# Performance work log

Hardware: AMD Instinct MI355X
Metric: run time of the kernel (lower is better)

Reference implementation:

```python
import jax, jax.numpy as jnp
import numpy as np

LATENT_DIM = 8
HALF = LATENT_DIM // 2
N_BLOCKS = 3
EPS = 1e-10


def _causal_graphs(koopman):
    # koopman: [C, D, D] real. Batched eig-decomp, band-pass eigenvalues by |lam| in [0.9, 1.1],
    # equivalent to selecting stable columns/rows: V_s diag(lam_s) V_s^-1 == V diag(lam*mask) V^-1.
    lam, V = jnp.linalg.eig(koopman)            # lam: [C,D] complex, V: [C,D,D]
    Vinv = jnp.linalg.inv(V)
    lam = lam + (1e-10 + 1e-10j)
    a = jnp.abs(lam)
    mask = (a <= 1.1) & (a >= 0.9)              # [C,D]
    # fallback: if no stable eigenvalue in a group, keep all (torch.arange branch)
    mask = jnp.where(jnp.any(mask, axis=-1, keepdims=True), mask, True)
    lam_m = lam * mask.astype(lam.dtype)
    G = jnp.einsum('cij,cj,cjk->cik', V, lam_m, Vinv)
    return jnp.real(G).astype(koopman.dtype)    # [C,D,D]


def _coupling(x, cond, W0, b0, W1, b1, W2, b2):
    # Conditional affine coupling flow: x,cond [..., D]. Returns (z, logdet [...])
    logdet = jnp.zeros(x.shape[:-1], dtype=x.dtype)
    for i in range(N_BLOCKS):
        x1, x2 = x[..., :HALF], x[..., HALF:]
        if i % 2 == 1:
            x1, x2 = x2, x1
        h = jnp.concatenate([x1, cond], axis=-1)            # [..., HALF + D]
        h = jax.nn.relu(h @ W0[i] + b0[i])
        h = jax.nn.relu(h @ W1[i] + b1[i])
        o = h @ W2[i] + b2[i]                               # [..., 2*HALF]
        s = jnp.tanh(o[..., :HALF])
        t = o[..., HALF:]
        x2 = x2 * jnp.exp(s) + t
        logdet = logdet + jnp.sum(s, axis=-1)
        if i % 2 == 1:
            x1, x2 = x2, x1
        x = jnp.concatenate([x1, x2], axis=-1)
    return x, logdet


def _std_normal_logprob(z):
    # standard MVN log prob, summed over last dim
    D = z.shape[-1]
    c = jnp.asarray(0.5 * D * np.log(2.0 * np.pi), dtype=z.dtype)
    return -0.5 * jnp.sum(z * z, axis=-1) - c


def setup_inputs() -> dict:
    key = jax.random.key(0)
    ks = jax.random.split(key, 9)
    B, N, T, D, C, H = 32, 4096, 16, LATENT_DIM, 32, 64
    latent = jax.random.normal(ks[0], (B, N, T, D), dtype=jnp.float32)
    # scale so eigenvalue magnitudes cluster near ~1 (spectral radius of D x D gaussian ~ 0.35*sqrt(D))
    koopman_tilde = jax.random.normal(ks[1], (C, D, D), dtype=jnp.float32) * 0.35
    community = jax.random.normal(ks[2], (N, C), dtype=jnp.float32)
    s0 = 1.0 / np.sqrt(HALF + D)
    s1 = 1.0 / np.sqrt(H)
    W0 = jax.random.normal(ks[3], (N_BLOCKS, HALF + D, H), dtype=jnp.float32) * s0
    b0 = jnp.zeros((N_BLOCKS, H), dtype=jnp.float32)
    W1 = jax.random.normal(ks[4], (N_BLOCKS, H, H), dtype=jnp.float32) * s1
    b1 = jnp.zeros((N_BLOCKS, H), dtype=jnp.float32)
    W2 = jax.random.normal(ks[5], (N_BLOCKS, H, 2 * HALF), dtype=jnp.float32) * s1
    b2 = jnp.zeros((N_BLOCKS, 2 * HALF), dtype=jnp.float32)
    return {"latent": latent, "koopman_tilde": koopman_tilde, "community": community,
            "W0": W0, "b0": b0, "W1": W1, "b1": b1, "W2": W2, "b2": b2}


def reference(latent, koopman_tilde, community, W0, b0, W1, b1, W2, b2):
    # scale_type == 'community' branch
    community_class = jnp.argmax(community, axis=-1)        # [N], topk k=1 indices
    graphs = _causal_graphs(koopman_tilde)                  # [C, D, D]
    G_node = graphs[community_class]                        # [N, D, D] gather per node
    # dispatch/matmul/combine fused as one einsum (parent[:, class==i] = latent[:, class==i] @ G_i)
    parent = jnp.einsum('bntd,nde->bnte', latent, G_node)
    ez, logdet = _coupling(latent, parent, W0, b0, W1, b1, W2, b2)
    log_pz = _std_normal_logprob(ez) + logdet               # [B, N, T]
    return log_pz
```

## Files before the change

kernel.cpp:

```cpp
#include <hip/hip_runtime.h>
#include <hip/hip_bf16.h>

typedef __attribute__((ext_vector_type(8))) short     bf16x8;
typedef __attribute__((ext_vector_type(4))) float     f32x4;
typedef __attribute__((ext_vector_type(4))) unsigned  u32x4;

__device__ inline unsigned short bf16_rn(float x) {
  unsigned u = __float_as_uint(x);
  unsigned r = (u + 0x7FFFu + ((u >> 16) & 1u)) >> 16;
  return (unsigned short)r;
}
__device__ inline unsigned cvt_pk_bf16(float a, float b) {
  unsigned r;
  asm("v_cvt_pk_bf16_f32 %0, %1, %2" : "=v"(r) : "v"(a), "v"(b));
  return r;
}
__device__ inline void pin4f(f32x4& v) { asm("" : "+v"(v)); }
__device__ inline void pin4u(u32x4& v) { asm("" : "+v"(v)); }
__device__ inline void wfence() {
  asm volatile("s_waitcnt lgkmcnt(0)" ::: "memory");
}
__device__ inline float tanh_fast(float v) {
  float vv = fminf(fmaxf(v, -15.f), 15.f);
  float e = __expf(2.f * vv);
  return (e - 1.f) * __builtin_amdgcn_rcpf(e + 1.f);
}

__global__ __launch_bounds__(256) void prologue_kernel(
    const float* __restrict__ Kt, const float* __restrict__ comm,
    const float* __restrict__ W0, const float* __restrict__ W1,
    const float* __restrict__ W2,
    float* __restrict__ Gout, int* __restrict__ cls,
    unsigned* __restrict__ wfrag)
{
  const int b = blockIdx.x;
  const int t = threadIdx.x;

  if (b < 32) {
    __shared__ double Kd[64];
    __shared__ double Pw[2][64];
    __shared__ double psum[8];
    __shared__ double coefs[9];
    __shared__ double rts[16];
    __shared__ double Gpart[64][8];

    const int tl = t & 63;
    const int row = tl >> 3, col = tl & 7;

    if (t < 64) Kd[tl] = (double)Kt[b * 64 + tl];
    __syncthreads();
    if (t < 64) Pw[0][tl] = Kd[tl];
    __syncthreads();

    int cur = 0;
    for (int p = 1; p <= 8; ++p) {
      if (t == 0) {
        double tr = 0.0;
        for (int d = 0; d < 8; ++d) tr += Pw[cur][d * 9];
        psum[p - 1] = tr;
      }
      if (p < 8 && t < 64) {
        double sacc = 0.0;
        for (int k = 0; k < 8; ++k) sacc += Pw[cur][row * 8 + k] * Kd[k * 8 + col];
        Pw[cur ^ 1][tl] = sacc;
      }
      __syncthreads();
      cur ^= 1;
    }

    if (t == 0) {
      double a[9];
      a[0] = 1.0;
      for (int k = 1; k <= 8; ++k) {
        double ssum = psum[k - 1];
        for (int i = 1; i < k; ++i) ssum += a[i] * psum[k - i - 1];
        a[k] = -ssum / (double)k;
      }
      for (int k = 0; k <= 8; ++k) coefs[k] = a[k];
    }
    __syncthreads();

    if (t < 8) {
      double a8[9];
      #pragma unroll
      for (int k = 0; k <= 8; ++k) a8[k] = coefs[k];
      double zre = 1.0, zim = 0.0;
      for (int q = 0; q <= t; ++q) {
        double t1 = zre * 0.4 - zim * 0.9;
        double t2 = zre * 0.9 + zim * 0.4;
        zre = t1; zim = t2;
      }
      for (int it = 0; it < 40; ++it) {
        double pre = a8[0], pim = 0.0;
        #pragma unroll
        for (int k = 1; k <= 8; ++k) {
          double t1 = pre * zre - pim * zim + a8[k];
          double t2 = pre * zim + pim * zre;
          pre = t1; pim = t2;
        }
        double dre = 1.0, dim = 0.0;
        for (int j = 0; j < 8; ++j) {
          double ore = __shfl(zre, j, 64);
          double oim = __shfl(zim, j, 64);
          if (j != t) {
            double sre = zre - ore, sim = zim - oim;
            double t1 = dre * sre - dim * sim;
            double t2 = dre * sim + dim * sre;
            dre = t1; dim = t2;
          }
        }
        double d2 = dre * dre + dim * dim;
        if (d2 < 1e-60) d2 = 1e-60;
        double qre = (pre * dre + pim * dim) / d2;
        double qim = (pim * dre - pre * dim) / d2;
        zre -= qre; zim -= qim;
      }
      rts[t] = zre; rts[8 + t] = zim;
    }
    __syncthreads();

    if (t < 64) {
      double lre[8], lim[8];
      #pragma unroll
      for (int j = 0; j < 8; ++j) { lre[j] = rts[j]; lim[j] = rts[8 + j]; }

      bool keep[8]; bool any = false;
      #pragma unroll
      for (int j = 0; j < 8; ++j) {
        double sre = lre[j] + 1e-10, sim = lim[j] + 1e-10;
        double amod = sqrt(sre * sre + sim * sim);
        keep[j] = (amod <= 1.1) && (amod >= 0.9);
        any = any || keep[j];
      }
      #pragma unroll
      for (int j = 0; j < 8; ++j) if (!any) keep[j] = true;

      const int r = tl >> 3, myrow = tl & 7;
      const int first = (r == 0) ? 1 : 0;
      double vre[8], vim[8];
      #pragma unroll
      for (int cc = 0; cc < 8; ++cc) {
        vre[cc] = Kd[myrow * 8 + cc] - ((myrow == cc) ? lre[first] : 0.0);
        vim[cc] = (myrow == cc) ? -lim[first] : 0.0;
      }
      #pragma unroll
      for (int j = 0; j < 8; ++j) {
        if (j == r || j == first) continue;
        double nre[8], nim[8];
        #pragma unroll
        for (int cc = 0; cc < 8; ++cc) {
          double are = 0.0, aim = 0.0;
          #pragma unroll
          for (int k = 0; k < 8; ++k) {
            double bre = Kd[k * 8 + cc] - ((k == cc) ? lre[j] : 0.0);
            double bim = (k == cc) ? -lim[j] : 0.0;
            are += vre[k] * bre - vim[k] * bim;
            aim += vre[k] * bim + vim[k] * bre;
          }
          nre[cc] = are; nim[cc] = aim;
        }
        #pragma unroll
        for (int cc = 0; cc < 8; ++cc) { vre[cc] = nre[cc]; vim[cc] = nim[cc]; }
      }

      double dre = 1.0, dim = 0.0;
      #pragma unroll
      for (int j = 0; j < 8; ++j) {
        if (j == r) continue;
        double ure = lre[r] - lre[j], uim = lim[r] - lim[j];
        double t1 = dre * ure - dim * uim;
        double t2 = dre * uim + dim * ure;
        dre = t1; dim = t2;
      }
      double numre = keep[r] ? (lre[r] + 1e-10) : 0.0;
      double numim = keep[r] ? (lim[r] + 1e-10) : 0.0;
      double dd = dre * dre + dim * dim;
      if (dd < 1e-300) dd = 1e-300;
      double cre = (numre * dre + numim * dim) / dd;
      double cim = (numim * dre - numre * dim) / dd;

      #pragma unroll
      for (int cc = 0; cc < 8; ++cc)
        Gpart[tl][cc] = cre * vre[cc] - cim * vim[cc];
    }
    __syncthreads();

    if (t < 64) {
      double sum = 0.0;
      #pragma unroll
      for (int rr = 0; rr < 8; ++rr) sum += Gpart[rr * 8 + (t >> 3)][t & 7];
      Gout[b * 64 + t] = (float)sum;
    }
    return;
  }

  if (b < 48) {
    int n = (b - 32) * 256 + t;
    if (n < 4096) {
      const float* rowp = comm + n * 32;
      float best = rowp[0];
      int bi = 0;
      #pragma unroll
      for (int c = 1; c < 32; ++c) {
        float v = rowp[c];
        if (v > best) { best = v; bi = c; }
      }
      cls[n] = bi;
    }
    return;
  }

  {
    int gid = (b - 48) * 256 + t;
    if (gid >= 42 * 64) return;
    int fid = gid >> 6, lane = gid & 63;
    int i = fid / 14, fl = fid % 14;
    int c = lane & 15, g = lane >> 4;

    unsigned short vals[8];
    #pragma unroll
    for (int j = 0; j < 8; ++j) {
      float v = 0.f;
      if (fl < 4) {
        int nb = fl;
        int k = 8 * g + j;
        if (k < 12) v = W0[i * 768 + k * 64 + 16 * nb + c];
      } else if (fl < 12) {
        int q = fl - 4; int kb = q >> 2, nb = q & 3;
        int k = 32 * kb + 16 * ((j >> 2) & 1) + 4 * g + 2 * ((j >> 1) & 1) + (j & 1);
        v = W1[i * 4096 + k * 64 + 16 * nb + c];
      } else {
        int kb = fl - 12;
        int k = 32 * kb + 16 * ((j >> 2) & 1) + 4 * g + 2 * ((j >> 1) & 1) + (j & 1);
        if (c < 8) v = W2[i * 512 + k * 8 + c];
      }
      vals[j] = bf16_rn(v);
    }
    u32x4 o;
    #pragma unroll
    for (int tt = 0; tt < 4; ++tt)
      o[tt] = (unsigned)vals[2 * tt] | ((unsigned)vals[2 * tt + 1] << 16);
    *(u32x4*)(wfrag + fid * 256 + lane * 4) = o;
  }
}

#define SPB 256

__global__ __launch_bounds__(256, 2) void causal_mfma_kernel(
    const float* __restrict__ latent, const float* __restrict__ graphs,
    const int* __restrict__ cls, const unsigned* __restrict__ wfrag,
    const float* __restrict__ b0, const float* __restrict__ b1,
    const float* __restrict__ b2, float* __restrict__ out)
{
  __shared__ unsigned wsh[42 * 256];
  __shared__ float    bsh[408];
  __shared__ char     ex[4][2048];

  const int t = threadIdx.x;
  const int lane = t & 63;
  const int w = t >> 6;
  const int c = lane & 15;
  const int g = lane >> 4;
  const int s = blockIdx.x * SPB + t;
  char* my = ex[w];

  #pragma unroll
  for (int q = 0; q < 11; ++q) {
    int idx = q * 256 + t;
    if (idx < 42 * 64)
      *(u32x4*)(wsh + idx * 4) = *(const u32x4*)(wfrag + idx * 4);
  }
  for (int idx = t; idx < 408; idx += 256) {
    bsh[idx] = (idx < 192) ? b0[idx] : (idx < 384) ? b1[idx - 192] : b2[idx - 384];
  }

  float x[8];
  {
    const float4 xa = *(const float4*)(latent + (size_t)s * 8);
    const float4 xb = *(const float4*)(latent + (size_t)s * 8 + 4);
    x[0] = xa.x; x[1] = xa.y; x[2] = xa.z; x[3] = xa.w;
    x[4] = xb.x; x[5] = xb.y; x[6] = xb.z; x[7] = xb.w;
  }
  unsigned parP0, parP1;
  u32x4 hi4;
  {
    float par[8];
    const int n = (s >> 4) & 4095;
    const float* G = graphs + cls[n] * 64;
    #pragma unroll
    for (int e = 0; e < 8; ++e) par[e] = 0.f;
    #pragma unroll
    for (int d = 0; d < 8; ++d) {
      const float xd = x[d];
      const float4 g0 = *(const float4*)(G + d * 8);
      const float4 g1 = *(const float4*)(G + d * 8 + 4);
      par[0] += xd * g0.x; par[1] += xd * g0.y; par[2] += xd * g0.z; par[3] += xd * g0.w;
      par[4] += xd * g1.x; par[5] += xd * g1.y; par[6] += xd * g1.z; par[7] += xd * g1.w;
    }
    parP0 = cvt_pk_bf16(par[0], par[1]);
    parP1 = cvt_pk_bf16(par[2], par[3]);
    hi4[0] = cvt_pk_bf16(par[4], par[5]);
    hi4[1] = cvt_pk_bf16(par[6], par[7]);
    hi4[2] = 0u; hi4[3] = 0u;
  }

  __syncthreads();

  const char* wl = (const char*)wsh + lane * 16;
  char* a_u  = my + lane * 32;
  char* a_b0 = my + (c)      * 32 + g * 16;
  char* a_b1 = my + (16 + c) * 32 + g * 16;
  char* a_b2 = my + (32 + c) * 32 + g * 16;
  char* a_b3 = my + (48 + c) * 32 + g * 16;

  float logdet = 0.f;

  #pragma unroll
  for (int i = 0; i < 3; ++i) {
    const int in0 = (i & 1) ? 4 : 0;
    const int tr0 = (i & 1) ? 0 : 4;
    const char* wbase = wl + (size_t)(i * 14) * 1024;

    {
      u32x4 lo4;
      lo4[0] = cvt_pk_bf16(x[in0], x[in0 + 1]);
      lo4[1] = cvt_pk_bf16(x[in0 + 2], x[in0 + 3]);
      lo4[2] = parP0; lo4[3] = parP1;
      wfence();
      *(u32x4*)a_u = lo4;
      *(u32x4*)(a_u + 16) = hi4;
      wfence();
    }

    u32x4 B1[4];
    {
      u32x4 z = {0u, 0u, 0u, 0u};
      B1[0] = (g < 2) ? *(const u32x4*)a_b0 : z;
      B1[1] = (g < 2) ? *(const u32x4*)a_b1 : z;
      B1[2] = (g < 2) ? *(const u32x4*)a_b2 : z;
      B1[3] = (g < 2) ? *(const u32x4*)a_b3 : z;
      pin4u(B1[0]); pin4u(B1[1]); pin4u(B1[2]); pin4u(B1[3]);
    }

    u32x4 B2k0[4], B2k1[4];
    {
      f32x4 a0[4], a1[4];
      bf16x8 A0 = *(const bf16x8*)(wbase + 0 * 1024);
      bf16x8 A1 = *(const bf16x8*)(wbase + 1 * 1024);
      f32x4 bv0 = *(const f32x4*)(bsh + i * 64 + 0 * 16 + g * 4);
      f32x4 bv1 = *(const f32x4*)(bsh + i * 64 + 1 * 16 + g * 4);
      #pragma unroll
      for (int mb = 0; mb < 4; ++mb) {
        a0[mb] = __builtin_amdgcn_mfma_f32_16x16x32_bf16(
            A0, __builtin_bit_cast(bf16x8, B1[mb]), bv0, 0, 0, 0);
        pin4f(a0[mb]);
      }
      #pragma unroll
      for (int mb = 0; mb < 4; ++mb) {
        a1[mb] = __builtin_amdgcn_mfma_f32_16x16x32_bf16(
            A1, __builtin_bit_cast(bf16x8, B1[mb]), bv1, 0, 0, 0);
        pin4f(a1[mb]);
      }
      #pragma unroll
      for (int mb = 0; mb < 4; ++mb) {
        B2k0[mb] = u32x4{cvt_pk_bf16(fmaxf(a0[mb][0], 0.f), fmaxf(a0[mb][1], 0.f)),
                         cvt_pk_bf16(fmaxf(a0[mb][2], 0.f), fmaxf(a0[mb][3], 0.f)),
                         cvt_pk_bf16(fmaxf(a1[mb][0], 0.f), fmaxf(a1[mb][1], 0.f)),
                         cvt_pk_bf16(fmaxf(a1[mb][2], 0.f), fmaxf(a1[mb][3], 0.f))};
        pin4u(B2k0[mb]);
      }
    }
    {
      f32x4 a0[4], a1[4];
      bf16x8 A0 = *(const bf16x8*)(wbase + 2 * 1024);
      bf16x8 A1 = *(const bf16x8*)(wbase + 3 * 1024);
      f32x4 bv0 = *(const f32x4*)(bsh + i * 64 + 2 * 16 + g * 4);
      f32x4 bv1 = *(const f32x4*)(bsh + i * 64 + 3 * 16 + g * 4);
      #pragma unroll
      for (int mb = 0; mb < 4; ++mb) {
        a0[mb] = __builtin_amdgcn_mfma_f32_16x16x32_bf16(
            A0, __builtin_bit_cast(bf16x8, B1[mb]), bv0, 0, 0, 0);
        pin4f(a0[mb]);
      }
      #pragma unroll
      for (int mb = 0; mb < 4; ++mb) {
        a1[mb] = __builtin_amdgcn_mfma_f32_16x16x32_bf16(
            A1, __builtin_bit_cast(bf16x8, B1[mb]), bv1, 0, 0, 0);
        pin4f(a1[mb]);
      }
      #pragma unroll
      for (int mb = 0; mb < 4; ++mb) {
        B2k1[mb] = u32x4{cvt_pk_bf16(fmaxf(a0[mb][0], 0.f), fmaxf(a0[mb][1], 0.f)),
                         cvt_pk_bf16(fmaxf(a0[mb][2], 0.f), fmaxf(a0[mb][3], 0.f)),
                         cvt_pk_bf16(fmaxf(a1[mb][0], 0.f), fmaxf(a1[mb][1], 0.f)),
                         cvt_pk_bf16(fmaxf(a1[mb][2], 0.f), fmaxf(a1[mb][3], 0.f))};
        pin4u(B2k1[mb]);
      }
    }

    u32x4 B3k0[4], B3k1[4];
    {
      f32x4 a0[4], a1[4];
      bf16x8 Ak0n0 = *(const bf16x8*)(wbase + (4 + 0) * 1024);
      bf16x8 Ak0n1 = *(const bf16x8*)(wbase + (4 + 1) * 1024);
      bf16x8 Ak1n0 = *(const bf16x8*)(wbase + (8 + 0) * 1024);
      bf16x8 Ak1n1 = *(const bf16x8*)(wbase + (8 + 1) * 1024);
      f32x4 bv0 = *(const f32x4*)(bsh + 192 + i * 64 + 0 * 16 + g * 4);
      f32x4 bv1 = *(const f32x4*)(bsh + 192 + i * 64 + 1 * 16 + g * 4);
      #pragma unroll
      for (int mb = 0; mb < 4; ++mb) {
        a0[mb] = __builtin_amdgcn_mfma_f32_16x16x32_bf16(
            Ak0n0, __builtin_bit_cast(bf16x8, B2k0[mb]), bv0, 0, 0, 0);
        a0[mb] = __builtin_amdgcn_mfma_f32_16x16x32_bf16(
            Ak1n0, __builtin_bit_cast(bf16x8, B2k1[mb]), a0[mb], 0, 0, 0);
        pin4f(a0[mb]);
      }
      #pragma unroll
      for (int mb = 0; mb < 4; ++mb) {
        a1[mb] = __builtin_amdgcn_mfma_f32_16x16x32_bf16(
            Ak0n1, __builtin_bit_cast(bf16x8, B2k0[mb]), bv1, 0, 0, 0);
        a1[mb] = __builtin_amdgcn_mfma_f32_16x16x32_bf16(
            Ak1n1, __builtin_bit_cast(bf16x8, B2k1[mb]), a1[mb], 0, 0, 0);
        pin4f(a1[mb]);
      }
      #pragma unroll
      for (int mb = 0; mb < 4; ++mb) {
        B3k0[mb] = u32x4{cvt_pk_bf16(fmaxf(a0[mb][0], 0.f), fmaxf(a0[mb][1], 0.f)),
                         cvt_pk_bf16(fmaxf(a0[mb][2], 0.f), fmaxf(a0[mb][3], 0.f)),
                         cvt_pk_bf16(fmaxf(a1[mb][0], 0.f), fmaxf(a1[mb][1], 0.f)),
                         cvt_pk_bf16(fmaxf(a1[mb][2], 0.f), fmaxf(a1[mb][3], 0.f))};
        pin4u(B3k0[mb]);
      }
    }
    {
      f32x4 a0[4], a1[4];
      bf16x8 Ak0n2 = *(const bf16x8*)(wbase + (4 + 2) * 1024);
      bf16x8 Ak0n3 = *(const bf16x8*)(wbase + (4 + 3) * 1024);
      bf16x8 Ak1n2 = *(const bf16x8*)(wbase + (8 + 2) * 1024);
      bf16x8 Ak1n3 = *(const bf16x8*)(wbase + (8 + 3) * 1024);
      f32x4 bv0 = *(const f32x4*)(bsh + 192 + i * 64 + 2 * 16 + g * 4);
      f32x4 bv1 = *(const f32x4*)(bsh + 192 + i * 64 + 3 * 16 + g * 4);
      #pragma unroll
      for (int mb = 0; mb < 4; ++mb) {
        a0[mb] = __builtin_amdgcn_mfma_f32_16x16x32_bf16(
            Ak0n2, __builtin_bit_cast(bf16x8, B2k0[mb]), bv0, 0, 0, 0);
        a0[mb] = __builtin_amdgcn_mfma_f32_16x16x32_bf16(
            Ak1n2, __builtin_bit_cast(bf16x8, B2k1[mb]), a0[mb], 0, 0, 0);
        pin4f(a0[mb]);
      }
      #pragma unroll
      for (int mb = 0; mb < 4; ++mb) {
        a1[mb] = __builtin_amdgcn_mfma_f32_16x16x32_bf16(
            Ak0n3, __builtin_bit_cast(bf16x8, B2k0[mb]), bv1, 0, 0, 0);
        a1[mb] = __builtin_amdgcn_mfma_f32_16x16x32_bf16(
            Ak1n3, __builtin_bit_cast(bf16x8, B2k1[mb]), a1[mb], 0, 0, 0);
        pin4f(a1[mb]);
      }
      #pragma unroll
      for (int mb = 0; mb < 4; ++mb) {
        B3k1[mb] = u32x4{cvt_pk_bf16(fmaxf(a0[mb][0], 0.f), fmaxf(a0[mb][1], 0.f)),
                         cvt_pk_bf16(fmaxf(a0[mb][2], 0.f), fmaxf(a0[mb][3], 0.f)),
                         cvt_pk_bf16(fmaxf(a1[mb][0], 0.f), fmaxf(a1[mb][1], 0.f)),
                         cvt_pk_bf16(fmaxf(a1[mb][2], 0.f), fmaxf(a1[mb][3], 0.f))};
        pin4u(B3k1[mb]);
      }
    }

    f32x4 acc3[4];
    {
      bf16x8 A0 = *(const bf16x8*)(wbase + 12 * 1024);
      bf16x8 A1 = *(const bf16x8*)(wbase + 13 * 1024);
      f32x4 z = {0.f, 0.f, 0.f, 0.f};
      f32x4 bC2 = (g < 2) ? *(const f32x4*)(bsh + 384 + i * 8 + g * 4) : z;
      #pragma unroll
      for (int mb = 0; mb < 4; ++mb) {
        f32x4 tmp = __builtin_amdgcn_mfma_f32_16x16x32_bf16(
            A0, __builtin_bit_cast(bf16x8, B3k0[mb]), bC2, 0, 0, 0);
        acc3[mb] = __builtin_amdgcn_mfma_f32_16x16x32_bf16(
            A1, __builtin_bit_cast(bf16x8, B3k1[mb]), tmp, 0, 0, 0);
        pin4f(acc3[mb]);
      }
    }

    wfence();
    if (g < 2) {
      *(u32x4*)a_b0 = __builtin_bit_cast(u32x4, acc3[0]);
      *(u32x4*)a_b1 = __builtin_bit_cast(u32x4, acc3[1]);
      *(u32x4*)a_b2 = __builtin_bit_cast(u32x4, acc3[2]);
      *(u32x4*)a_b3 = __builtin_bit_cast(u32x4, acc3[3]);
    }
    wfence();

    {
      u32x4 o0 = *(const u32x4*)a_u;
      u32x4 o1 = *(const u32x4*)(a_u + 16);
      float sv0 = tanh_fast(__uint_as_float(o0[0]));
      float sv1 = tanh_fast(__uint_as_float(o0[1]));
      float sv2 = tanh_fast(__uint_as_float(o0[2]));
      float sv3 = tanh_fast(__uint_as_float(o0[3]));
      x[tr0 + 0] = x[tr0 + 0] * __expf(sv0) + __uint_as_float(o1[0]);
      x[tr0 + 1] = x[tr0 + 1] * __expf(sv1) + __uint_as_float(o1[1]);
      x[tr0 + 2] = x[tr0 + 2] * __expf(sv2) + __uint_as_float(o1[2]);
      x[tr0 + 3] = x[tr0 + 3] * __expf(sv3) + __uint_as_float(o1[3]);
      logdet += sv0 + sv1 + sv2 + sv3;
    }
  }

  float ss = 0.f;
  #pragma unroll
  for (int q = 0; q < 8; ++q) ss += x[q] * x[q];
  out[s] = -0.5f * ss - 7.3515082656373810f + logdet;
}

extern "C" void kernel_launch(void* const* d_in, const int* in_sizes, int n_in,
                              void* d_out, int out_size, void* d_ws, size_t ws_size,
                              hipStream_t stream) {
  const float* latent  = (const float*)d_in[0];
  const float* koopman = (const float*)d_in[1];
  const float* comm    = (const float*)d_in[2];
  const float* W0      = (const float*)d_in[3];
  const float* b0      = (const float*)d_in[4];
  const float* W1      = (const float*)d_in[5];
  const float* b1      = (const float*)d_in[6];
  const float* W2      = (const float*)d_in[7];
  const float* b2      = (const float*)d_in[8];
  float* out = (float*)d_out;

  float*    graphs_ws = (float*)d_ws;
  int*      cls_ws    = (int*)((char*)d_ws + 8192);
  unsigned* wfrag_ws  = (unsigned*)((char*)d_ws + 24576);

  prologue_kernel<<<59, 256, 0, stream>>>(
      koopman, comm, W0, W1, W2, graphs_ws, cls_ws, wfrag_ws);

  const int total = 32 * 4096 * 16;
  causal_mfma_kernel<<<total / SPB, SPB, 0, stream>>>(
      latent, graphs_ws, cls_ws, wfrag_ws, b0, b1, b2, out);
}
```

Before: 149.9 us.

## Process two sample tiles per thread to interleave independent MFMA chains

Each 256-thread block now handles 512 samples: every thread carries two independent samples through the three coupling blocks, with a second per-wave LDS exchange buffer. MFMA calls for the two tiles are interleaved so the dependent accumulate chains overlap, weight fragments loaded from LDS are reused across both tiles, and the per-block weight staging cost is spread over twice the work. In exchange register pressure roughly doubles, which at launch bounds (256,2) risks spills, and the grid shrinks by half.

```diff
diff --git a/kernel.cpp b/kernel.cpp
--- a/kernel.cpp
+++ b/kernel.cpp
@@ -24,6 +24,9 @@
   float vv = fminf(fmaxf(v, -15.f), 15.f);
   float e = __expf(2.f * vv);
   return (e - 1.f) * __builtin_amdgcn_rcpf(e + 1.f);
+}
+__device__ inline unsigned rp(float a, float b) {
+  return cvt_pk_bf16(fmaxf(a, 0.f), fmaxf(b, 0.f));
 }
 
 __global__ __launch_bounds__(256) void prologue_kernel(
@@ -244,7 +247,7 @@
   }
 }
 
-#define SPB 256
+#define SPB 512
 
 __global__ __launch_bounds__(256, 2) void causal_mfma_kernel(
     const float* __restrict__ latent, const float* __restrict__ graphs,
@@ -254,15 +257,18 @@
 {
   __shared__ unsigned wsh[42 * 256];
   __shared__ float    bsh[408];
-  __shared__ char     ex[4][2048];
+  __shared__ char     ex0[4][2048];
+  __shared__ char     ex1[4][2048];
 
   const int t = threadIdx.x;
   const int lane = t & 63;
   const int w = t >> 6;
   const int c = lane & 15;
   const int g = lane >> 4;
-  const int s = blockIdx.x * SPB + t;
-  char* my = ex[w];
+  const int s0 = blockIdx.x * SPB + t;
+  const int s1 = s0 + 256;
+  char* my0 = ex0[w];
+  char* my1 = ex1[w];
 
   #pragma unroll
   for (int q = 0; q < 11; ++q) {
@@ -274,46 +280,73 @@
     bsh[idx] = (idx < 192) ? b0[idx] : (idx < 384) ? b1[idx - 192] : b2[idx - 384];
   }
 
-  float x[8];
+  float xA[8], xB[8];
   {
-    const float4 xa = *(const float4*)(latent + (size_t)s * 8);
-    const float4 xb = *(const float4*)(latent + (size_t)s * 8 + 4);
-    x[0] = xa.x; x[1] = xa.y; x[2] = xa.z; x[3] = xa.w;
-    x[4] = xb.x; x[5] = xb.y; x[6] = xb.z; x[7] = xb.w;
-  }
-  unsigned parP0, parP1;
-  u32x4 hi4;
+    const float4 a0 = *(const float4*)(latent + (size_t)s0 * 8);
+    const float4 a1 = *(const float4*)(latent + (size_t)s0 * 8 + 4);
+    xA[0] = a0.x; xA[1] = a0.y; xA[2] = a0.z; xA[3] = a0.w;
+    xA[4] = a1.x; xA[5] = a1.y; xA[6] = a1.z; xA[7] = a1.w;
+    const float4 b0v = *(const float4*)(latent + (size_t)s1 * 8);
+    const float4 b1v = *(const float4*)(latent + (size_t)s1 * 8 + 4);
+    xB[0] = b0v.x; xB[1] = b0v.y; xB[2] = b0v.z; xB[3] = b0v.w;
+    xB[4] = b1v.x; xB[5] = b1v.y; xB[6] = b1v.z; xB[7] = b1v.w;
+  }
+  unsigned pA0, pA1, pB0, pB1;
+  u32x4 hiA, hiB;
   {
     float par[8];
-    const int n = (s >> 4) & 4095;
-    const float* G = graphs + cls[n] * 64;
+    const float* G = graphs + cls[(s0 >> 4) & 4095] * 64;
     #pragma unroll
     for (int e = 0; e < 8; ++e) par[e] = 0.f;
     #pragma unroll
     for (int d = 0; d < 8; ++d) {
-      const float xd = x[d];
+      const float xd = xA[d];
       const float4 g0 = *(const float4*)(G + d * 8);
       const float4 g1 = *(const float4*)(G + d * 8 + 4);
       par[0] += xd * g0.x; par[1] += xd * g0.y; par[2] += xd * g0.z; par[3] += xd * g0.w;
       par[4] += xd * g1.x; par[5] += xd * g1.y; par[6] += xd * g1.z; par[7] += xd * g1.w;
     }
-    parP0 = cvt_pk_bf16(par[0], par[1]);
-    parP1 = cvt_pk_bf16(par[2], par[3]);
-    hi4[0] = cvt_pk_bf16(par[4], par[5]);
-    hi4[1] = cvt_pk_bf16(par[6], par[7]);
-    hi4[2] = 0u; hi4[3] = 0u;
+    pA0 = cvt_pk_bf16(par[0], par[1]);
+    pA1 = cvt_pk_bf16(par[2], par[3]);
+    hiA[0] = cvt_pk_bf16(par[4], par[5]);
+    hiA[1] = cvt_pk_bf16(par[6], par[7]);
+    hiA[2] = 0u; hiA[3] = 0u;
+  }
+  {
+    float par[8];
+    const float* G = graphs + cls[(s1 >> 4) & 4095] * 64;
+    #pragma unroll
+    for (int e = 0; e < 8; ++e) par[e] = 0.f;
+    #pragma unroll
+    for (int d = 0; d < 8; ++d) {
+      const float xd = xB[d];
+      const float4 g0 = *(const float4*)(G + d * 8);
+      const float4 g1 = *(const float4*)(G + d * 8 + 4);
+      par[0] += xd * g0.x; par[1] += xd * g0.y; par[2] += xd * g0.z; par[3] += xd * g0.w;
+      par[4] += xd * g1.x; par[5] += xd * g1.y; par[6] += xd * g1.z; par[7] += xd * g1.w;
+    }
+    pB0 = cvt_pk_bf16(par[0], par[1]);
+    pB1 = cvt_pk_bf16(par[2], par[3]);
+    hiB[0] = cvt_pk_bf16(par[4], par[5]);
+    hiB[1] = cvt_pk_bf16(par[6], par[7]);
+    hiB[2] = 0u; hiB[3] = 0u;
   }
 
   __syncthreads();
 
   const char* wl = (const char*)wsh + lane * 16;
-  char* a_u  = my + lane * 32;
-  char* a_b0 = my + (c)      * 32 + g * 16;
-  char* a_b1 = my + (16 + c) * 32 + g * 16;
-  char* a_b2 = my + (32 + c) * 32 + g * 16;
-  char* a_b3 = my + (48 + c) * 32 + g * 16;
-
-  float logdet = 0.f;
+  char* aA_u  = my0 + lane * 32;
+  char* aA_b0 = my0 + (c)      * 32 + g * 16;
+  char* aA_b1 = my0 + (16 + c) * 32 + g * 16;
+  char* aA_b2 = my0 + (32 + c) * 32 + g * 16;
+  char* aA_b3 = my0 + (48 + c) * 32 + g * 16;
+  char* aB_u  = my1 + lane * 32;
+  char* aB_b0 = my1 + (c)      * 32 + g * 16;
+  char* aB_b1 = my1 + (16 + c) * 32 + g * 16;
+  char* aB_b2 = my1 + (32 + c) * 32 + g * 16;
+  char* aB_b3 = my1 + (48 + c) * 32 + g * 16;
+
+  float logdetA = 0.f, logdetB = 0.f;
 
   #pragma unroll
   for (int i = 0; i < 3; ++i) {
@@ -322,151 +355,197 @@
     const char* wbase = wl + (size_t)(i * 14) * 1024;
 
     {
-      u32x4 lo4;
-      lo4[0] = cvt_pk_bf16(x[in0], x[in0 + 1]);
-      lo4[1] = cvt_pk_bf16(x[in0 + 2], x[in0 + 3]);
-      lo4[2] = parP0; lo4[3] = parP1;
+      u32x4 loA, loB;
+      loA[0] = cvt_pk_bf16(xA[in0], xA[in0 + 1]);
+      loA[1] = cvt_pk_bf16(xA[in0 + 2], xA[in0 + 3]);
+      loA[2] = pA0; loA[3] = pA1;
+      loB[0] = cvt_pk_bf16(xB[in0], xB[in0 + 1]);
+      loB[1] = cvt_pk_bf16(xB[in0 + 2], xB[in0 + 3]);
+      loB[2] = pB0; loB[3] = pB1;
       wfence();
-      *(u32x4*)a_u = lo4;
-      *(u32x4*)(a_u + 16) = hi4;
+      *(u32x4*)aA_u = loA;
+      *(u32x4*)(aA_u + 16) = hiA;
+      *(u32x4*)aB_u = loB;
+      *(u32x4*)(aB_u + 16) = hiB;
       wfence();
     }
 
-    u32x4 B1[4];
+    u32x4 B1A[4], B1B[4];
     {
       u32x4 z = {0u, 0u, 0u, 0u};
-      B1[0] = (g < 2) ? *(const u32x4*)a_b0 : z;
-      B1[1] = (g < 2) ? *(const u32x4*)a_b1 : z;
-      B1[2] = (g < 2) ? *(const u32x4*)a_b2 : z;
-      B1[3] = (g < 2) ? *(const u32x4*)a_b3 : z;
-      pin4u(B1[0]); pin4u(B1[1]); pin4u(B1[2]); pin4u(B1[3]);
-    }
-
-    u32x4 B2k0[4], B2k1[4];
-    {
-      f32x4 a0[4], a1[4];
+      B1A[0] = (g < 2) ? *(const u32x4*)aA_b0 : z;
+      B1A[1] = (g < 2) ? *(const u32x4*)aA_b1 : z;
+      B1A[2] = (g < 2) ? *(const u32x4*)aA_b2 : z;
+      B1A[3] = (g < 2) ? *(const u32x4*)aA_b3 : z;
+      B1B[0] = (g < 2) ? *(const u32x4*)aB_b0 : z;
+      B1B[1] = (g < 2) ? *(const u32x4*)aB_b1 : z;
+      B1B[2] = (g < 2) ? *(const u32x4*)aB_b2 : z;
+      B1B[3] = (g < 2) ? *(const u32x4*)aB_b3 : z;
+      #pragma unroll
+      for (int mb = 0; mb < 4; ++mb) { pin4u(B1A[mb]); pin4u(B1B[mb]); }
+    }
+
+    u32x4 B2k0A[4], B2k1A[4], B2k0B[4], B2k1B[4];
+    {
       bf16x8 A0 = *(const bf16x8*)(wbase + 0 * 1024);
       bf16x8 A1 = *(const bf16x8*)(wbase + 1 * 1024);
       f32x4 bv0 = *(const f32x4*)(bsh + i * 64 + 0 * 16 + g * 4);
       f32x4 bv1 = *(const f32x4*)(bsh + i * 64 + 1 * 16 + g * 4);
-      #pragma unroll
-      for (int mb = 0; mb < 4; ++mb) {
-        a0[mb] = __builtin_amdgcn_mfma_f32_16x16x32_bf16(
-            A0, __builtin_bit_cast(bf16x8, B1[mb]), bv0, 0, 0, 0);
-        pin4f(a0[mb]);
-      }
-      #pragma unroll
-      for (int mb = 0; mb < 4; ++mb) {
-        a1[mb] = __builtin_amdgcn_mfma_f32_16x16x32_bf16(
-            A1, __builtin_bit_cast(bf16x8, B1[mb]), bv1, 0, 0, 0);
-        pin4f(a1[mb]);
-      }
-      #pragma unroll
-      for (int mb = 0; mb < 4; ++mb) {
-        B2k0[mb] = u32x4{cvt_pk_bf16(fmaxf(a0[mb][0], 0.f), fmaxf(a0[mb][1], 0.f)),
-                         cvt_pk_bf16(fmaxf(a0[mb][2], 0.f), fmaxf(a0[mb][3], 0.f)),
-                         cvt_pk_bf16(fmaxf(a1[mb][0], 0.f), fmaxf(a1[mb][1], 0.f)),
-                         cvt_pk_bf16(fmaxf(a1[mb][2], 0.f), fmaxf(a1[mb][3], 0.f))};
-        pin4u(B2k0[mb]);
-      }
-    }
-    {
-      f32x4 a0[4], a1[4];
+      f32x4 q0[4], q1[4], r0[4], r1[4];
+      #pragma unroll
+      for (int mb = 0; mb < 4; ++mb) {
+        q0[mb] = __builtin_amdgcn_mfma_f32_16x16x32_bf16(
+            A0, __builtin_bit_cast(bf16x8, B1A[mb]), bv0, 0, 0, 0);
+        pin4f(q0[mb]);
+        r0[mb] = __builtin_amdgcn_mfma_f32_16x16x32_bf16(
+            A0, __builtin_bit_cast(bf16x8, B1B[mb]), bv0, 0, 0, 0);
+        pin4f(r0[mb]);
+      }
+      #pragma unroll
+      for (int mb = 0; mb < 4; ++mb) {
+        q1[mb] = __builtin_amdgcn_mfma_f32_16x16x32_bf16(
+            A1, __builtin_bit_cast(bf16x8, B1A[mb]), bv1, 0, 0, 0);
+        pin4f(q1[mb]);
+        r1[mb] = __builtin_amdgcn_mfma_f32_16x16x32_bf16(
+            A1, __builtin_bit_cast(bf16x8, B1B[mb]), bv1, 0, 0, 0);
+        pin4f(r1[mb]);
+      }
+      #pragma unroll
+      for (int mb = 0; mb < 4; ++mb) {
+        B2k0A[mb] = u32x4{rp(q0[mb][0], q0[mb][1]), rp(q0[mb][2], q0[mb][3]),
+                          rp(q1[mb][0], q1[mb][1]), rp(q1[mb][2], q1[mb][3])};
+        pin4u(B2k0A[mb]);
+        B2k0B[mb] = u32x4{rp(r0[mb][0], r0[mb][1]), rp(r0[mb][2], r0[mb][3]),
+                          rp(r1[mb][0], r1[mb][1]), rp(r1[mb][2], r1[mb][3])};
+        pin4u(B2k0B[mb]);
+      }
+    }
+    {
       bf16x8 A0 = *(const bf16x8*)(wbase + 2 * 1024);
       bf16x8 A1 = *(const bf16x8*)(wbase + 3 * 1024);
       f32x4 bv0 = *(const f32x4*)(bsh + i * 64 + 2 * 16 + g * 4);
       f32x4 bv1 = *(const f32x4*)(bsh + i * 64 + 3 * 16 + g * 4);
-      #pragma unroll
-      for (int mb = 0; mb < 4; ++mb) {
-        a0[mb] = __builtin_amdgcn_mfma_f32_16x16x32_bf16(
-            A0, __builtin_bit_cast(bf16x8, B1[mb]), bv0, 0, 0, 0);
-        pin4f(a0[mb]);
-      }
-      #pragma unroll
-      for (int mb = 0; mb < 4; ++mb) {
-        a1[mb] = __builtin_amdgcn_mfma_f32_16x16x32_bf16(
-            A1, __builtin_bit_cast(bf16x8, B1[mb]), bv1, 0, 0, 0);
-        pin4f(a1[mb]);
-      }
-      #pragma unroll
-      for (int mb = 0; mb < 4; ++mb) {
-        B2k1[mb] = u32x4{cvt_pk_bf16(fmaxf(a0[mb][0], 0.f), fmaxf(a0[mb][1], 0.f)),
-                         cvt_pk_bf16(fmaxf(a0[mb][2], 0.f), fmaxf(a0[mb][3], 0.f)),
-                         cvt_pk_bf16(fmaxf(a1[mb][0], 0.f), fmaxf(a1[mb][1], 0.f)),
-                         cvt_pk_bf16(fmaxf(a1[mb][2], 0.f), fmaxf(a1[mb][3], 0.f))};
-        pin4u(B2k1[mb]);
-      }
-    }
-
-    u32x4 B3k0[4], B3k1[4];
-    {
-      f32x4 a0[4], a1[4];
+      f32x4 q0[4], q1[4], r0[4], r1[4];
+      #pragma unroll
+      for (int mb = 0; mb < 4; ++mb) {
+        q0[mb] = __builtin_amdgcn_mfma_f32_16x16x32_bf16(
+            A0, __builtin_bit_cast(bf16x8, B1A[mb]), bv0, 0, 0, 0);
+        pin4f(q0[mb]);
+        r0[mb] = __builtin_amdgcn_mfma_f32_16x16x32_bf16(
+            A0, __builtin_bit_cast(bf16x8, B1B[mb]), bv0, 0, 0, 0);
+        pin4f(r0[mb]);
+      }
+      #pragma unroll
+      for (int mb = 0; mb < 4; ++mb) {
+        q1[mb] = __builtin_amdgcn_mfma_f32_16x16x32_bf16(
+            A1, __builtin_bit_cast(bf16x8, B1A[mb]), bv1, 0, 0, 0);
+        pin4f(q1[mb]);
+        r1[mb] = __builtin_amdgcn_mfma_f32_16x16x32_bf16(
+            A1, __builtin_bit_cast(bf16x8, B1B[mb]), bv1, 0, 0, 0);
+        pin4f(r1[mb]);
+      }
+      #pragma unroll
+      for (int mb = 0; mb < 4; ++mb) {
+        B2k1A[mb] = u32x4{rp(q0[mb][0], q0[mb][1]), rp(q0[mb][2], q0[mb][3]),
+                          rp(q1[mb][0], q1[mb][1]), rp(q1[mb][2], q1[mb][3])};
+        pin4u(B2k1A[mb]);
+        B2k1B[mb] = u32x4{rp(r0[mb][0], r0[mb][1]), rp(r0[mb][2], r0[mb][3]),
+                          rp(r1[mb][0], r1[mb][1]), rp(r1[mb][2], r1[mb][3])};
+        pin4u(B2k1B[mb]);
+      }
+    }
+
+    u32x4 B3k0A[4], B3k1A[4], B3k0B[4], B3k1B[4];
+    {
       bf16x8 Ak0n0 = *(const bf16x8*)(wbase + (4 + 0) * 1024);
       bf16x8 Ak0n1 = *(const bf16x8*)(wbase + (4 + 1) * 1024);
       bf16x8 Ak1n0 = *(const bf16x8*)(wbase + (8 + 0) * 1024);
       bf16x8 Ak1n1 = *(const bf16x8*)(wbase + (8 + 1) * 1024);
       f32x4 bv0 = *(const f32x4*)(bsh + 192 + i * 64 + 0 * 16 + g * 4);
       f32x4 bv1 = *(const f32x4*)(bsh + 192 + i * 64 + 1 * 16 + g * 4);
-      #pragma unroll
-      for (int mb = 0; mb < 4; ++mb) {
-        a0[mb] = __builtin_amdgcn_mfma_f32_16x16x32_bf16(
-            Ak0n0, __builtin_bit_cast(bf16x8, B2k0[mb]), bv0, 0, 0, 0);
-        a0[mb] = __builtin_amdgcn_mfma_f32_16x16x32_bf16(
-            Ak1n0, __builtin_bit_cast(bf16x8, B2k1[mb]), a0[mb], 0, 0, 0);
-        pin4f(a0[mb]);
-      }
-      #pragma unroll
-      for (int mb = 0; mb < 4; ++mb) {
-        a1[mb] = __builtin_amdgcn_mfma_f32_16x16x32_bf16(
-            Ak0n1, __builtin_bit_cast(bf16x8, B2k0[mb]), bv1, 0, 0, 0);
-        a1[mb] = __builtin_amdgcn_mfma_f32_16x16x32_bf16(
-            Ak1n1, __builtin_bit_cast(bf16x8, B2k1[mb]), a1[mb], 0, 0, 0);
-        pin4f(a1[mb]);
-      }
-      #pragma unroll
-      for (int mb = 0; mb < 4; ++mb) {
-        B3k0[mb] = u32x4{cvt_pk_bf16(fmaxf(a0[mb][0], 0.f), fmaxf(a0[mb][1], 0.f)),
-                         cvt_pk_bf16(fmaxf(a0[mb][2], 0.f), fmaxf(a0[mb][3], 0.f)),
-                         cvt_pk_bf16(fmaxf(a1[mb][0], 0.f), fmaxf(a1[mb][1], 0.f)),
-                         cvt_pk_bf16(fmaxf(a1[mb][2], 0.f), fmaxf(a1[mb][3], 0.f))};
-        pin4u(B3k0[mb]);
-      }
-    }
-    {
-      f32x4 a0[4], a1[4];
+      f32x4 q0[4], q1[4], r0[4], r1[4];
+      #pragma unroll
+      for (int mb = 0; mb < 4; ++mb) {
+        q0[mb] = __builtin_amdgcn_mfma_f32_16x16x32_bf16(
+            Ak0n0, __builtin_bit_cast(bf16x8, B2k0A[mb]), bv0, 0, 0, 0);
+        q0[mb] = __builtin_amdgcn_mfma_f32_16x16x32_bf16(
+            Ak1n0, __builtin_bit_cast(bf16x8, B2k1A[mb]), q0[mb], 0, 0, 0);
+        pin4f(q0[mb]);
+        r0[mb] = __builtin_amdgcn_mfma_f32_16x16x32_bf16(
+            Ak0n0, __builtin_bit_cast(bf16x8, B2k0B[mb]), bv0, 0, 0, 0);
+        r0[mb] = __builtin_amdgcn_mfma_f32_16x16x32_bf16(
+            Ak1n0, __builtin_bit_cast(bf16x8, B2k1B[mb]), r0[mb], 0, 0, 0);
+        pin4f(r0[mb]);
+      }
+      #pragma unroll
+      for (int mb = 0; mb < 4; ++mb) {
+        q1[mb] = __builtin_amdgcn_mfma_f32_16x16x32_bf16(
+            Ak0n1, __builtin_bit_cast(bf16x8, B2k0A[mb]), bv1, 0, 0, 0);
+        q1[mb] = __builtin_amdgcn_mfma_f32_16x16x32_bf16(
+            Ak1n1, __builtin_bit_cast(bf16x8, B2k1A[mb]), q1[mb], 0, 0, 0);
+        pin4f(q1[mb]);
+        r1[mb] = __builtin_amdgcn_mfma_f32_16x16x32_bf16(
+            Ak0n1, __builtin_bit_cast(bf16x8, B2k0B[mb]), bv1, 0, 0, 0);
+        r1[mb] = __builtin_amdgcn_mfma_f32_16x16x32_bf16(
+            Ak1n1, __builtin_bit_cast(bf16x8, B2k1B[mb]), r1[mb], 0, 0, 0);
+        pin4f(r1[mb]);
+      }
+      #pragma unroll
+      for (int mb = 0; mb < 4; ++mb) {
+        B3k0A[mb] = u32x4{rp(q0[mb][0], q0[mb][1]), rp(q0[mb][2], q0[mb][3]),
+                          rp(q1[mb][0], q1[mb][1]), rp(q1[mb][2], q1[mb][3])};
+        pin4u(B3k0A[mb]);
+        B3k0B[mb] = u32x4{rp(r0[mb][0], r0[mb][1]), rp(r0[mb][2], r0[mb][3]),
+                          rp(r1[mb][0], r1[mb][1]), rp(r1[mb][2], r1[mb][3])};
+        pin4u(B3k0B[mb]);
+      }
+    }
+    {
       bf16x8 Ak0n2 = *(const bf16x8*)(wbase + (4 + 2) * 1024);
       bf16x8 Ak0n3 = *(const bf16x8*)(wbase + (4 + 3) * 1024);
       bf16x8 Ak1n2 = *(const bf16x8*)(wbase + (8 + 2) * 1024);
       bf16x8 Ak1n3 = *(const bf16x8*)(wbase + (8 + 3) * 1024);
       f32x4 bv0 = *(const f32x4*)(bsh + 192 + i * 64 + 2 * 16 + g * 4);
       f32x4 bv1 = *(const f32x4*)(bsh + 192 + i * 64 + 3 * 16 + g * 4);
-      #pragma unroll
-      for (int mb = 0; mb < 4; ++mb) {
-        a0[mb] = __builtin_amdgcn_mfma_f32_16x16x32_bf16(
-            Ak0n2, __builtin_bit_cast(bf16x8, B2k0[mb]), bv0, 0, 0, 0);
-        a0[mb] = __builtin_amdgcn_mfma_f32_16x16x32_bf16(
-            Ak1n2, __builtin_bit_cast(bf16x8, B2k1[mb]), a0[mb], 0, 0, 0);
-        pin4f(a0[mb]);
-      }
-      #pragma unroll
-      for (int mb = 0; mb < 4; ++mb) {
-        a1[mb] = __builtin_amdgcn_mfma_f32_16x16x32_bf16(
-            Ak0n3, __builtin_bit_cast(bf16x8, B2k0[mb]), bv1, 0, 0, 0);
-        a1[mb] = __builtin_amdgcn_mfma_f32_16x16x32_bf16(
-            Ak1n3, __builtin_bit_cast(bf16x8, B2k1[mb]), a1[mb], 0, 0, 0);
-        pin4f(a1[mb]);
-      }
-      #pragma unroll
-      for (int mb = 0; mb < 4; ++mb) {
-        B3k1[mb] = u32x4{cvt_pk_bf16(fmaxf(a0[mb][0], 0.f), fmaxf(a0[mb][1], 0.f)),
-                         cvt_pk_bf16(fmaxf(a0[mb][2], 0.f), fmaxf(a0[mb][3], 0.f)),
-                         cvt_pk_bf16(fmaxf(a1[mb][0], 0.f), fmaxf(a1[mb][1], 0.f)),
-                         cvt_pk_bf16(fmaxf(a1[mb][2], 0.f), fmaxf(a1[mb][3], 0.f))};
-        pin4u(B3k1[mb]);
-      }
-    }
-
-    f32x4 acc3[4];
+      f32x4 q0[4], q1[4], r0[4], r1[4];
+      #pragma unroll
+      for (int mb = 0; mb < 4; ++mb) {
+        q0[mb] = __builtin_amdgcn_mfma_f32_16x16x32_bf16(
+            Ak0n2, __builtin_bit_cast(bf16x8, B2k0A[mb]), bv0, 0, 0, 0);
+        q0[mb] = __builtin_amdgcn_mfma_f32_16x16x32_bf16(
+            Ak1n2, __builtin_bit_cast(bf16x8, B2k1A[mb]), q0[mb], 0, 0, 0);
+        pin4f(q0[mb]);
+        r0[mb] = __builtin_amdgcn_mfma_f32_16x16x32_bf16(
+            Ak0n2, __builtin_bit_cast(bf16x8, B2k0B[mb]), bv0, 0, 0, 0);
+        r0[mb] = __builtin_amdgcn_mfma_f32_16x16x32_bf16(
+            Ak1n2, __builtin_bit_cast(bf16x8, B2k1B[mb]), r0[mb], 0, 0, 0);
+        pin4f(r0[mb]);
+      }
+      #pragma unroll
+      for (int mb = 0; mb < 4; ++mb) {
+        q1[mb] = __builtin_amdgcn_mfma_f32_16x16x32_bf16(
+            Ak0n3, __builtin_bit_cast(bf16x8, B2k0A[mb]), bv1, 0, 0, 0);
+        q1[mb] = __builtin_amdgcn_mfma_f32_16x16x32_bf16(
+            Ak1n3, __builtin_bit_cast(bf16x8, B2k1A[mb]), q1[mb], 0, 0, 0);
+        pin4f(q1[mb]);
+        r1[mb] = __builtin_amdgcn_mfma_f32_16x16x32_bf16(
+            Ak0n3, __builtin_bit_cast(bf16x8, B2k0B[mb]), bv1, 0, 0, 0);
+        r1[mb] = __builtin_amdgcn_mfma_f32_16x16x32_bf16(
+            Ak1n3, __builtin_bit_cast(bf16x8, B2k1B[mb]), r1[mb], 0, 0, 0);
+        pin4f(r1[mb]);
+      }
+      #pragma unroll
+      for (int mb = 0; mb < 4; ++mb) {
+        B3k1A[mb] = u32x4{rp(q0[mb][0], q0[mb][1]), rp(q0[mb][2], q0[mb][3]),
+                          rp(q1[mb][0], q1[mb][1]), rp(q1[mb][2], q1[mb][3])};
+        pin4u(B3k1A[mb]);
+        B3k1B[mb] = u32x4{rp(r0[mb][0], r0[mb][1]), rp(r0[mb][2], r0[mb][3]),
+                          rp(r1[mb][0], r1[mb][1]), rp(r1[mb][2], r1[mb][3])};
+        pin4u(B3k1B[mb]);
+      }
+    }
+
+    f32x4 acc3A[4], acc3B[4];
     {
       bf16x8 A0 = *(const bf16x8*)(wbase + 12 * 1024);
       bf16x8 A1 = *(const bf16x8*)(wbase + 13 * 1024);
@@ -474,42 +553,63 @@
       f32x4 bC2 = (g < 2) ? *(const f32x4*)(bsh + 384 + i * 8 + g * 4) : z;
       #pragma unroll
       for (int mb = 0; mb < 4; ++mb) {
-        f32x4 tmp = __builtin_amdgcn_mfma_f32_16x16x32_bf16(
-            A0, __builtin_bit_cast(bf16x8, B3k0[mb]), bC2, 0, 0, 0);
-        acc3[mb] = __builtin_amdgcn_mfma_f32_16x16x32_bf16(
-            A1, __builtin_bit_cast(bf16x8, B3k1[mb]), tmp, 0, 0, 0);
-        pin4f(acc3[mb]);
+        f32x4 ta = __builtin_amdgcn_mfma_f32_16x16x32_bf16(
+            A0, __builtin_bit_cast(bf16x8, B3k0A[mb]), bC2, 0, 0, 0);
+        acc3A[mb] = __builtin_amdgcn_mfma_f32_16x16x32_bf16(
+            A1, __builtin_bit_cast(bf16x8, B3k1A[mb]), ta, 0, 0, 0);
+        pin4f(acc3A[mb]);
+        f32x4 tb = __builtin_amdgcn_mfma_f32_16x16x32_bf16(
+            A0, __builtin_bit_cast(bf16x8, B3k0B[mb]), bC2, 0, 0, 0);
+        acc3B[mb] = __builtin_amdgcn_mfma_f32_16x16x32_bf16(
+            A1, __builtin_bit_cast(bf16x8, B3k1B[mb]), tb, 0, 0, 0);
+        pin4f(acc3B[mb]);
       }
     }
 
     wfence();
     if (g < 2) {
-      *(u32x4*)a_b0 = __builtin_bit_cast(u32x4, acc3[0]);
-      *(u32x4*)a_b1 = __builtin_bit_cast(u32x4, acc3[1]);
-      *(u32x4*)a_b2 = __builtin_bit_cast(u32x4, acc3[2]);
-      *(u32x4*)a_b3 = __builtin_bit_cast(u32x4, acc3[3]);
+      *(u32x4*)aA_b0 = __builtin_bit_cast(u32x4, acc3A[0]);
+      *(u32x4*)aA_b1 = __builtin_bit_cast(u32x4, acc3A[1]);
+      *(u32x4*)aA_b2 = __builtin_bit_cast(u32x4, acc3A[2]);
+      *(u32x4*)aA_b3 = __builtin_bit_cast(u32x4, acc3A[3]);
+      *(u32x4*)aB_b0 = __builtin_bit_cast(u32x4, acc3B[0]);
+      *(u32x4*)aB_b1 = __builtin_bit_cast(u32x4, acc3B[1]);
+      *(u32x4*)aB_b2 = __builtin_bit_cast(u32x4, acc3B[2]);
+      *(u32x4*)aB_b3 = __builtin_bit_cast(u32x4, acc3B[3]);
     }
     wfence();
 
     {
-      u32x4 o0 = *(const u32x4*)a_u;
-      u32x4 o1 = *(const u32x4*)(a_u + 16);
-      float sv0 = tanh_fast(__uint_as_float(o0[0]));
-      float sv1 = tanh_fast(__uint_as_float(o0[1]));
-      float sv2 = tanh_fast(__uint_as_float(o0[2]));
-      float sv3 = tanh_fast(__uint_as_float(o0[3]));
-      x[tr0 + 0] = x[tr0 + 0] * __expf(sv0) + __uint_as_float(o1[0]);
-      x[tr0 + 1] = x[tr0 + 1] * __expf(sv1) + __uint_as_float(o1[1]);
-      x[tr0 + 2] = x[tr0 + 2] * __expf(sv2) + __uint_as_float(o1[2]);
-      x[tr0 + 3] = x[tr0 + 3] * __expf(sv3) + __uint_as_float(o1[3]);
-      logdet += sv0 + sv1 + sv2 + sv3;
-    }
-  }
-
-  float ss = 0.f;
+      u32x4 oA0 = *(const u32x4*)aA_u;
+      u32x4 oA1 = *(const u32x4*)(aA_u + 16);
+      u32x4 oB0 = *(const u32x4*)aB_u;
+      u32x4 oB1 = *(const u32x4*)(aB_u + 16);
+      float sA0 = tanh_fast(__uint_as_float(oA0[0]));
+      float sA1 = tanh_fast(__uint_as_float(oA0[1]));
+      float sA2 = tanh_fast(__uint_as_float(oA0[2]));
+      float sA3 = tanh_fast(__uint_as_float(oA0[3]));
+      xA[tr0 + 0] = xA[tr0 + 0] * __expf(sA0) + __uint_as_float(oA1[0]);
+      xA[tr0 + 1] = xA[tr0 + 1] * __expf(sA1) + __uint_as_float(oA1[1]);
+      xA[tr0 + 2] = xA[tr0 + 2] * __expf(sA2) + __uint_as_float(oA1[2]);
+      xA[tr0 + 3] = xA[tr0 + 3] * __expf(sA3) + __uint_as_float(oA1[3]);
+      logdetA += sA0 + sA1 + sA2 + sA3;
+      float sB0 = tanh_fast(__uint_as_float(oB0[0]));
+      float sB1 = tanh_fast(__uint_as_float(oB0[1]));
+      float sB2 = tanh_fast(__uint_as_float(oB0[2]));
+      float sB3 = tanh_fast(__uint_as_float(oB0[3]));
+      xB[tr0 + 0] = xB[tr0 + 0] * __expf(sB0) + __uint_as_float(oB1[0]);
+      xB[tr0 + 1] = xB[tr0 + 1] * __expf(sB1) + __uint_as_float(oB1[1]);
+      xB[tr0 + 2] = xB[tr0 + 2] * __expf(sB2) + __uint_as_float(oB1[2]);
+      xB[tr0 + 3] = xB[tr0 + 3] * __expf(sB3) + __uint_as_float(oB1[3]);
+      logdetB += sB0 + sB1 + sB2 + sB3;
+    }
+  }
+
+  float ssA = 0.f, ssB = 0.f;
   #pragma unroll
-  for (int q = 0; q < 8; ++q) ss += x[q] * x[q];
-  out[s] = -0.5f * ss - 7.3515082656373810f + logdet;
+  for (int q = 0; q < 8; ++q) { ssA += xA[q] * xA[q]; ssB += xB[q] * xB[q]; }
+  out[s0] = -0.5f * ssA - 7.3515082656373810f + logdetA;
+  out[s1] = -0.5f * ssB - 7.3515082656373810f + logdetB;
 }
 
 extern "C" void kernel_launch(void* const* d_in, const int* in_sizes, int n_in,
@@ -534,6 +634,6 @@
       koopman, comm, W0, W1, W2, graphs_ws, cls_ws, wfrag_ws);
 
   const int total = 32 * 4096 * 16;
-  causal_mfma_kernel<<<total / SPB, SPB, 0, stream>>>(
+  causal_mfma_kernel<<<total / SPB, 256, 0, stream>>>(
       latent, graphs_ws, cls_ws, wfrag_ws, b0, b1, b2, out);
 }
```

After: 159.8 us. +6.6%, slower.
